# Kernel tuning notes

Measured on AMD Instinct MI355X. Metric: run time of the kernel, lower is better.

Reference implementation:

```python
import jax, jax.numpy as jnp
import numpy as np

D_MODEL = 1024
NHEAD = 16
HEAD_DIM = D_MODEL // NHEAD
EPS = 1e-5


def layernorm(x, g, b):
    mu = jnp.mean(x, axis=-1, keepdims=True)
    var = jnp.mean(jnp.square(x - mu), axis=-1, keepdims=True)
    return (x - mu) * jax.lax.rsqrt(var + EPS) * g + b


def setup_inputs() -> dict:
    key = jax.random.key(0)
    ks = jax.random.split(key, 10)
    B, S, D = 8, 2048, D_MODEL
    s = 1.0 / np.sqrt(D)
    return {
        "x": jax.random.normal(ks[0], (B, S, D), dtype=jnp.float32),
        "wq": jax.random.normal(ks[1], (D, D), dtype=jnp.float32) * s,
        "wk": jax.random.normal(ks[2], (D, D), dtype=jnp.float32) * s,
        "wv": jax.random.normal(ks[3], (D, D), dtype=jnp.float32) * s,
        "ln1_g": jnp.ones((D,), dtype=jnp.float32),
        "ln1_b": jnp.zeros((D,), dtype=jnp.float32),
        "ln2_g": jnp.ones((D,), dtype=jnp.float32),
        "ln2_b": jnp.zeros((D,), dtype=jnp.float32),
        "w1": jax.random.normal(ks[4], (D, D), dtype=jnp.float32) * s,
        "b1": jnp.zeros((D,), dtype=jnp.float32),
        "w2": jax.random.normal(ks[5], (D, D), dtype=jnp.float32) * s,
        "b2": jnp.zeros((D,), dtype=jnp.float32),
    }


def reference(x, wq, wk, wv, ln1_g, ln1_b, ln2_g, ln2_b, w1, b1, w2, b2):
    B, S, D = x.shape
    H, Dh = NHEAD, HEAD_DIM
    xn = layernorm(x, ln1_g, ln1_b)
    # nn.Linear: y = x @ W.T (no bias for q/k/v)
    q = (xn @ wq.T).reshape(B, S, H, Dh)
    k = (xn @ wk.T).reshape(B, S, H, Dh)
    v = (xn @ wv.T).reshape(B, S, H, Dh)
    scale = 1.0 / jnp.sqrt(jnp.float32(Dh))
    scores = jnp.einsum("bqhd,bkhd->bhqk", q, k) * scale  # [B,H,S,S]
    attn = jax.nn.softmax(scores, axis=-1)
    att = jnp.einsum("bhqk,bkhd->bqhd", attn, v).reshape(B, S, D)
    xt = layernorm(xn + att, ln2_g, ln2_b)
    ffn = jax.nn.relu(xt @ w1.T + b1) @ w2.T + b2
    return xt + ffn
```

## Files before the change

kernel.cpp:

```cpp
#include <hip/hip_runtime.h>
#include <hip/hip_bf16.h>

typedef __bf16 bf16x8 __attribute__((ext_vector_type(8)));
typedef float f32x4 __attribute__((ext_vector_type(4)));
typedef float f32x16 __attribute__((ext_vector_type(16)));

#define MFMA_B16(a, b, c) __builtin_amdgcn_mfma_f32_16x16x32_bf16((a), (b), (c), 0, 0, 0)
#define MFMA32_B16(a, b, c) __builtin_amdgcn_mfma_f32_32x32x16_bf16((a), (b), (c), 0, 0, 0)
#define GLD16(g, l)                                                              \
    __builtin_amdgcn_global_load_lds((__attribute__((address_space(1))) void*)(g), \
                                     (__attribute__((address_space(3))) void*)(l), \
                                     16, 0, 0)

__device__ __forceinline__ float bfu2f(unsigned short u) {
    return __uint_as_float(((unsigned)u) << 16);
}
__device__ __forceinline__ unsigned short f2bfu(float f) {
    unsigned u = __float_as_uint(f);
    u += 0x7fffu + ((u >> 16) & 1u);
    return (unsigned short)(u >> 16);
}
__device__ __forceinline__ float fexp2(float x) {
#if __has_builtin(__builtin_amdgcn_exp2f)
    return __builtin_amdgcn_exp2f(x);
#else
    return __expf(x * 0.69314718f);
#endif
}
__device__ __forceinline__ unsigned cvtpk_bf16(float lo_, float hi_) {
    unsigned r;
    asm("v_cvt_pk_bf16_f32 %0, %1, %2" : "=v"(r) : "v"(lo_), "v"(hi_));
    return r;
}
__device__ __forceinline__ void plswap(unsigned& a, unsigned& b) {
#if __has_builtin(__builtin_amdgcn_permlane32_swap)
    typedef int v2i __attribute__((ext_vector_type(2)));
    v2i r = __builtin_amdgcn_permlane32_swap((int)a, (int)b, false, false);
    a = (unsigned)r.x;
    b = (unsigned)r.y;
#else
    unsigned pa_ = (unsigned)__shfl_xor((int)a, 32);
    unsigned pb_ = (unsigned)__shfl_xor((int)b, 32);
    bool hi = (threadIdx.x & 63) >= 32;
    unsigned na = hi ? pb_ : a;
    unsigned nb = hi ? b : pa_;
    a = na;
    b = nb;
#endif
}

__global__ __launch_bounds__(256) void cvt5_f32_bf16(const float* __restrict__ s0,
                                                     const float* __restrict__ s1,
                                                     const float* __restrict__ s2,
                                                     const float* __restrict__ s3,
                                                     const float* __restrict__ s4,
                                                     unsigned short* __restrict__ dst) {
    int wsel = blockIdx.x >> 10;
    int i = (blockIdx.x & 1023) * 256 + threadIdx.x;
    const float* src = s0;
    if (wsel == 1) src = s1;
    else if (wsel == 2) src = s2;
    else if (wsel == 3) src = s3;
    else if (wsel == 4) src = s4;
    float4 v = ((const float4*)src)[i];
    ((ushort4*)dst)[wsel * 262144 + i] =
        make_ushort4(f2bfu(v.x), f2bfu(v.y), f2bfu(v.z), f2bfu(v.w));
}

__global__ __launch_bounds__(256) void ln1_kernel(const float* __restrict__ in1,
                                                  const float* __restrict__ gam,
                                                  const float* __restrict__ bet,
                                                  unsigned short* __restrict__ outb) {
    int row = blockIdx.x, tid = threadIdx.x;
    size_t base = (size_t)row * 1024 + tid * 4;
    float4 v = *(const float4*)(in1 + base);
    float s = v.x + v.y + v.z + v.w;
    float sq = v.x * v.x + v.y * v.y + v.z * v.z + v.w * v.w;
#pragma unroll
    for (int m = 1; m < 64; m <<= 1) {
        s += __shfl_xor(s, m);
        sq += __shfl_xor(sq, m);
    }
    __shared__ float red[8];
    int w = tid >> 6;
    if ((tid & 63) == 0) { red[w] = s; red[w + 4] = sq; }
    __syncthreads();
    s = red[0] + red[1] + red[2] + red[3];
    sq = red[4] + red[5] + red[6] + red[7];
    float mean = s * (1.0f / 1024.0f);
    float var = fmaxf(sq * (1.0f / 1024.0f) - mean * mean, 0.0f);
    float rstd = rsqrtf(var + 1e-5f);
    float4 g4 = *(const float4*)(gam + tid * 4);
    float4 b4 = *(const float4*)(bet + tid * 4);
    *(ushort4*)(outb + base) = make_ushort4(
        f2bfu((v.x - mean) * rstd * g4.x + b4.x), f2bfu((v.y - mean) * rstd * g4.y + b4.y),
        f2bfu((v.z - mean) * rstd * g4.z + b4.z), f2bfu((v.w - mean) * rstd * g4.w + b4.w));
}

__global__ __launch_bounds__(256) void ln2_kernel(const unsigned short* __restrict__ in1,
                                                  const unsigned short* __restrict__ in2,
                                                  const float* __restrict__ gam,
                                                  const float* __restrict__ bet,
                                                  unsigned short* __restrict__ outb) {
    int row = blockIdx.x, tid = threadIdx.x;
    size_t base = (size_t)row * 1024 + tid * 4;
    ushort4 a = *(const ushort4*)(in1 + base);
    ushort4 c = *(const ushort4*)(in2 + base);
    float4 v = make_float4(bfu2f(a.x) + bfu2f(c.x), bfu2f(a.y) + bfu2f(c.y),
                           bfu2f(a.z) + bfu2f(c.z), bfu2f(a.w) + bfu2f(c.w));
    float s = v.x + v.y + v.z + v.w;
    float sq = v.x * v.x + v.y * v.y + v.z * v.z + v.w * v.w;
#pragma unroll
    for (int m = 1; m < 64; m <<= 1) {
        s += __shfl_xor(s, m);
        sq += __shfl_xor(sq, m);
    }
    __shared__ float red[8];
    int w = tid >> 6;
    if ((tid & 63) == 0) { red[w] = s; red[w + 4] = sq; }
    __syncthreads();
    s = red[0] + red[1] + red[2] + red[3];
    sq = red[4] + red[5] + red[6] + red[7];
    float mean = s * (1.0f / 1024.0f);
    float var = fmaxf(sq * (1.0f / 1024.0f) - mean * mean, 0.0f);
    float rstd = rsqrtf(var + 1e-5f);
    float4 g4 = *(const float4*)(gam + tid * 4);
    float4 b4 = *(const float4*)(bet + tid * 4);
    *(ushort4*)(outb + base) = make_ushort4(
        f2bfu((v.x - mean) * rstd * g4.x + b4.x), f2bfu((v.y - mean) * rstd * g4.y + b4.y),
        f2bfu((v.z - mean) * rstd * g4.z + b4.z), f2bfu((v.w - mean) * rstd * g4.w + b4.w));
}

template <int MODE>
__global__ __launch_bounds__(512, 2) void gemm8(const unsigned short* __restrict__ A,
                                                const unsigned short* __restrict__ Bw,
                                                const float* __restrict__ bias,
                                                const unsigned short* __restrict__ resid,
                                                void* __restrict__ O0, void* __restrict__ O1,
                                                void* __restrict__ O2, int M, int N, int K) {
    __shared__ unsigned short As[4][8192];
    __shared__ unsigned short Bs[4][8192];
    int nt = N >> 8;
    int bid = blockIdx.x;
    int nwg = gridDim.x;
    int swz = (bid & 7) * (nwg >> 3) + (bid >> 3);
    int mt = swz / nt, ntl = swz % nt;
    int mbase = mt << 8, nbase = ntl << 8;
    int tid = threadIdx.x;
    int w = tid >> 6, l = tid & 63;
    int wm = w >> 2, wn = w & 3;
    int lr = l & 15, lg = l >> 4;
    int lx = lr & 7;
    int brow = (wn & 1) * 64;

    int srow = tid >> 3;
    int csrc = (tid & 7) ^ (srow & 7);
    const unsigned short* aRow = A + (size_t)(mbase + srow) * K + csrc * 8;
    const unsigned short* bRow = Bw + (size_t)(nbase + srow) * K + csrc * 8;

    const int NT = K >> 6;
    auto stA = [&](int buf, int h, int t) {
        if (t >= NT) return;
        const unsigned short* s0 = aRow + (size_t)(h * 128) * K + t * 64;
        GLD16(s0, &As[buf * 2 + h][w * 512]);
        GLD16(s0 + (size_t)64 * K, &As[buf * 2 + h][4096 + w * 512]);
    };
    auto stB = [&](int buf, int h, int t) {
        if (t >= NT) return;
        const unsigned short* s0 = bRow + (size_t)(h * 128) * K + t * 64;
        GLD16(s0, &Bs[buf * 2 + h][w * 512]);
        GLD16(s0 + (size_t)64 * K, &Bs[buf * 2 + h][4096 + w * 512]);
    };

    f32x4 acc[8][4] = {};
    bf16x8 afr[4][2], bq0[2][2], bq1[2][2];

    auto rdA = [&](int buf, int mq) {
        const unsigned short* base = &As[buf * 2 + wm][0];
#pragma unroll
        for (int mf = 0; mf < 4; mf++)
#pragma unroll
            for (int ks = 0; ks < 2; ks++)
                afr[mf][ks] = *(const bf16x8*)(base + (mq * 64 + mf * 16 + lr) * 64 +
                                               (((ks * 4 + lg) ^ lx) << 3));
    };
    auto rdB = [&](int buf, int nq, bf16x8 (&bf)[2][2]) {
        const unsigned short* base = &Bs[buf * 2 + (wn >> 1)][0];
#pragma unroll
        for (int nf = 0; nf < 2; nf++)
#pragma unroll
            for (int ks = 0; ks < 2; ks++)
                bf[nf][ks] = *(const bf16x8*)(base + (brow + nq * 32 + nf * 16 + lr) * 64 +
                                              (((ks * 4 + lg) ^ lx) << 3));
    };
    auto MM = [&](int mq, int nq, bf16x8 (&bf)[2][2]) {
        __builtin_amdgcn_s_setprio(1);
#pragma unroll
        for (int mf = 0; mf < 4; mf++)
#pragma unroll
            for (int nf = 0; nf < 2; nf++)
#pragma unroll
                for (int ks = 0; ks < 2; ks++)
                    acc[mq * 4 + mf][nq * 2 + nf] =
                        MFMA_B16(afr[mf][ks], bf[nf][ks], acc[mq * 4 + mf][nq * 2 + nf]);
        __builtin_amdgcn_s_setprio(0);
    };
#define BARX __builtin_amdgcn_s_barrier()
#define LGK0 do { asm volatile("s_waitcnt lgkmcnt(0)" ::: "memory"); \
                  __builtin_amdgcn_sched_barrier(0); } while (0)
#define VMC(n) asm volatile("s_waitcnt vmcnt(" #n ")" ::: "memory")

    stA(0, 0, 0); stA(0, 1, 0); stB(0, 0, 0); stB(0, 1, 0); stB(1, 0, 1); stB(1, 1, 1);
    VMC(4);
    BARX;

    int NIT = NT >> 1;
    for (int i = 0; i < NIT; i++) {
        int t0 = 2 * i, t1 = t0 + 1;
        bool lastI = (i == NIT - 1);
        rdA(0, 0); rdB(0, 0, bq0); stA(1, 0, t1);
        BARX; LGK0; MM(0, 0, bq0); BARX;
        rdB(0, 1, bq1); stA(1, 1, t1);
        BARX; LGK0; MM(0, 1, bq1); BARX;
        rdA(0, 1); stB(0, 0, t0 + 2);
        BARX; LGK0; MM(1, 1, bq1); BARX;
        stB(0, 1, t0 + 2);
        if (lastI) { VMC(0); } else { VMC(4); }
        BARX; MM(1, 0, bq0); BARX;
        rdA(1, 0); rdB(1, 0, bq0); stA(0, 0, t0 + 2);
        BARX; LGK0; MM(0, 0, bq0); BARX;
        rdB(1, 1, bq1); stA(0, 1, t0 + 2);
        BARX; LGK0; MM(0, 1, bq1); BARX;
        rdA(1, 1); stB(1, 0, t1 + 2);
        BARX; LGK0; MM(1, 1, bq1); BARX;
        stB(1, 1, t1 + 2);
        if (!lastI) { VMC(4); }
        BARX; MM(1, 0, bq0); BARX;
    }

#pragma unroll
    for (int m = 0; m < 8; m++) {
        int row = mbase + wm * 128 + (m >> 2) * 64 + (m & 3) * 16 + lg * 4;
#pragma unroll
        for (int n = 0; n < 4; n++) {
            int col = nbase + wn * 64 + (n >> 1) * 32 + (n & 1) * 16 + lr;
            if constexpr (MODE == 0) {
                int wsel = col >> 10;
                int cl = col & 1023;
                if (wsel == 2) {
                    int hh = cl >> 6, dd = cl & 63;
                    int bb = row >> 11, ss = row & 2047;
                    unsigned short t4[4];
#pragma unroll
                    for (int j = 0; j < 4; j++) t4[j] = f2bfu(acc[m][n][j]);
                    size_t vtidx = ((size_t)((bb * 16 + hh) * 64 + dd)) * 2048 + ss;
                    *(uint2*)((unsigned short*)O2 + vtidx) = *(uint2*)t4;
                } else {
                    unsigned short* out = (wsel == 0) ? (unsigned short*)O0 : (unsigned short*)O1;
                    float sc = (wsel == 0) ? 0.18033688f : 1.0f;
#pragma unroll
                    for (int j = 0; j < 4; j++)
                        out[(size_t)(row + j) * 1024 + cl] = f2bfu(acc[m][n][j] * sc);
                }
            } else {
                float bv = bias[col];
#pragma unroll
                for (int j = 0; j < 4; j++) {
                    float v = acc[m][n][j] + bv;
                    size_t idx = (size_t)(row + j) * N + col;
                    if constexpr (MODE == 1) {
                        ((unsigned short*)O0)[idx] = f2bfu(fmaxf(v, 0.0f));
                    } else {
                        ((float*)O0)[idx] = v + bfu2f(resid[idx]);
                    }
                }
            }
        }
    }
#undef BARX
#undef LGK0
#undef VMC
}

__global__ __launch_bounds__(512) void attn_kernel(const unsigned short* __restrict__ qq,
                                                   const unsigned short* __restrict__ kk,
                                                   const unsigned short* __restrict__ vT,
                                                   unsigned short* __restrict__ attb) {
    __shared__ unsigned short Ks[2][64 * 64];
    __shared__ unsigned short Vs[2][64 * 64];

    int bid = blockIdx.x;
    int swz = (bid & 7) * (gridDim.x >> 3) + (bid >> 3);
    int qi = swz & 7, h = (swz >> 3) & 15, b = swz >> 7;
    int tid = threadIdx.x, w = tid >> 6, l = tid & 63;
    int lo = l & 31, hi = l >> 5;
    int q0 = qi * 256 + w * 32;

    const unsigned short* qp = qq + ((size_t)((b * 2048 + q0 + lo) * 16 + h)) * 64 + hi * 8;
    bf16x8 qf[4];
#pragma unroll
    for (int kc = 0; kc < 4; kc++) qf[kc] = *(const bf16x8*)(qp + kc * 16);

    int srow = w * 8 + (l >> 3);
    int schunk = (l & 7) ^ ((l >> 3) & 7);
    const unsigned short* ksrc = kk + ((size_t)((b * 2048 + srow) * 16 + h)) * 64 + schunk * 8;
    const unsigned short* vsrc = vT + ((size_t)((b * 16 + h) * 64 + srow)) * 2048 + schunk * 8;

    f32x16 od0 = {}, od1 = {};
    float ssum = 0.f;

    GLD16(ksrc, &Ks[0][w * 512]);
    GLD16(vsrc, &Vs[0][w * 512]);
    ksrc += 65536;
    vsrc += 64;
    asm volatile("s_waitcnt vmcnt(0)");
    __syncthreads();

    int cur = 0;
    for (int t = 0; t < 32; t++) {
        if (t < 31) {
            GLD16(ksrc, &Ks[cur ^ 1][w * 512]);
            GLD16(vsrc, &Vs[cur ^ 1][w * 512]);
            ksrc += 65536;
            vsrc += 64;
        }
        const unsigned short* Kb = &Ks[cur][0];
        f32x16 sacc[2];
        __builtin_amdgcn_s_setprio(1);
#pragma unroll
        for (int tt = 0; tt < 2; tt++) {
            f32x16 s = {};
            int row = tt * 32 + lo;
#pragma unroll
            for (int kc = 0; kc < 4; kc++) {
                bf16x8 a = *(const bf16x8*)(Kb + row * 64 + (((kc * 2 + hi) ^ (row & 7)) << 3));
                s = MFMA32_B16(a, qf[kc], s);
            }
            sacc[tt] = s;
        }
        __builtin_amdgcn_s_setprio(0);
        float p[32];
        float psum = 0.f;
#pragma unroll
        for (int tt = 0; tt < 2; tt++)
#pragma unroll
            for (int r = 0; r < 16; r++) {
                float e = fexp2(sacc[tt][r]);
                p[tt * 16 + r] = e;
                psum += e;
            }
        psum += __shfl_xor(psum, 32);
        ssum += psum;
        const unsigned short* Vb = &Vs[cur][0];
#pragma unroll
        for (int tt = 0; tt < 2; tt++) {
            unsigned wv[8];
#pragma unroll
            for (int i = 0; i < 8; i++) wv[i] = cvtpk_bf16(p[tt * 16 + 2 * i], p[tt * 16 + 2 * i + 1]);
            plswap(wv[0], wv[2]);
            plswap(wv[1], wv[3]);
            plswap(wv[4], wv[6]);
            plswap(wv[5], wv[7]);
            union { unsigned u[4]; bf16x8 v; } c0, c1;
            c0.u[0] = wv[0]; c0.u[1] = wv[1]; c0.u[2] = wv[2]; c0.u[3] = wv[3];
            c1.u[0] = wv[4]; c1.u[1] = wv[5]; c1.u[2] = wv[6]; c1.u[3] = wv[7];
            __builtin_amdgcn_s_setprio(1);
#pragma unroll
            for (int sub = 0; sub < 2; sub++) {
                int ks = tt * 2 + sub;
                bf16x8 pa = sub ? c1.v : c0.v;
                int slot = ((ks * 2 + hi) ^ (lo & 7)) << 3;
                bf16x8 v0 = *(const bf16x8*)(Vb + lo * 64 + slot);
                bf16x8 v1 = *(const bf16x8*)(Vb + (32 + lo) * 64 + slot);
                od0 = MFMA32_B16(pa, v0, od0);
                od1 = MFMA32_B16(pa, v1, od1);
            }
            __builtin_amdgcn_s_setprio(0);
        }
        asm volatile("s_waitcnt vmcnt(0)");
        __syncthreads();
        cur ^= 1;
    }

#pragma unroll
    for (int r = 0; r < 16; r++) {
        int crow = (r & 3) + ((r >> 2) << 3) + (hi << 2);
        float rs = 1.0f / __shfl(ssum, crow);
        int q = q0 + crow;
        size_t base = ((size_t)((b * 2048 + q) * 16 + h)) * 64;
        attb[base + lo] = f2bfu(od0[r] * rs);
        attb[base + 32 + lo] = f2bfu(od1[r] * rs);
    }
}

extern "C" void kernel_launch(void* const* d_in, const int* in_sizes, int n_in,
                              void* d_out, int out_size, void* d_ws, size_t ws_size,
                              hipStream_t stream) {
    const float* x = (const float*)d_in[0];
    const float* wq = (const float*)d_in[1];
    const float* wk = (const float*)d_in[2];
    const float* wv = (const float*)d_in[3];
    const float* ln1_g = (const float*)d_in[4];
    const float* ln1_b = (const float*)d_in[5];
    const float* ln2_g = (const float*)d_in[6];
    const float* ln2_b = (const float*)d_in[7];
    const float* w1 = (const float*)d_in[8];
    const float* b1 = (const float*)d_in[9];
    const float* w2 = (const float*)d_in[10];
    const float* b2 = (const float*)d_in[11];

    const size_t NB = 33554432;
    char* ws = (char*)d_ws;
    unsigned short* xn_b = (unsigned short*)(ws);
    unsigned short* q_b = (unsigned short*)(ws + NB);
    unsigned short* k_b = (unsigned short*)(ws + 2 * NB);
    unsigned short* vT_b = (unsigned short*)(ws + 3 * NB);
    unsigned short* att_b = (unsigned short*)(ws + 4 * NB);
    unsigned short* wq_b = (unsigned short*)(ws + 5 * NB);
    unsigned short* w1_b = wq_b + 3145728;
    unsigned short* w2_b = w1_b + 1048576;
    unsigned short* xt_b = q_b;
    unsigned short* h_b = k_b;

    dim3 blk(256);
    cvt5_f32_bf16<<<5120, blk, 0, stream>>>(wq, wk, wv, w1, w2, wq_b);
    ln1_kernel<<<16384, blk, 0, stream>>>(x, ln1_g, ln1_b, xn_b);

    gemm8<0><<<768, dim3(512), 0, stream>>>(xn_b, wq_b, nullptr, nullptr,
                                            q_b, k_b, vT_b, 16384, 3072, 1024);

    attn_kernel<<<1024, dim3(512), 0, stream>>>(q_b, k_b, vT_b, att_b);

    ln2_kernel<<<16384, blk, 0, stream>>>(xn_b, att_b, ln2_g, ln2_b, xt_b);

    gemm8<1><<<256, dim3(512), 0, stream>>>(xt_b, w1_b, b1, nullptr,
                                            h_b, nullptr, nullptr, 16384, 1024, 1024);
    gemm8<2><<<256, dim3(512), 0, stream>>>(h_b, w2_b, b2, xt_b,
                                            d_out, nullptr, nullptr, 16384, 1024, 1024);
}
```

Measured before the change: 394.6 us.

## Deepen attention K/V prefetch to a 4-stage ring and stagger wave pairs

Replaces the double-buffered K/V LDS tiles in the attention kernel with a 4-deep ring that prefetches three tiles ahead. The old per-step full drain (vmcnt(0) plus syncthreads) becomes a partial vmcnt wait and a raw barrier. Odd waves work one tile ahead of even waves, wrapping to tile 0 at the end. This spreads MFMA and exp phases and LDS traffic across the wave pairs, and load latency is hidden deeper. In exchange the kernel doubles its LDS footprint and adds an extra barrier per step. The exp row-sum is also split into two accumulators to add ILP.

```diff
diff --git a/kernel.cpp b/kernel.cpp
--- a/kernel.cpp
+++ b/kernel.cpp
@@ -286,14 +286,15 @@
                                                    const unsigned short* __restrict__ kk,
                                                    const unsigned short* __restrict__ vT,
                                                    unsigned short* __restrict__ attb) {
-    __shared__ unsigned short Ks[2][64 * 64];
-    __shared__ unsigned short Vs[2][64 * 64];
+    __shared__ unsigned short Ks[4][64 * 64];
+    __shared__ unsigned short Vs[4][64 * 64];
 
     int bid = blockIdx.x;
     int swz = (bid & 7) * (gridDim.x >> 3) + (bid >> 3);
     int qi = swz & 7, h = (swz >> 3) & 15, b = swz >> 7;
     int tid = threadIdx.x, w = tid >> 6, l = tid & 63;
     int lo = l & 31, hi = l >> 5;
+    int g = w & 1;
     int q0 = qi * 256 + w * 32;
 
     const unsigned short* qp = qq + ((size_t)((b * 2048 + q0 + lo) * 16 + h)) * 64 + hi * 8;
@@ -303,55 +304,60 @@
 
     int srow = w * 8 + (l >> 3);
     int schunk = (l & 7) ^ ((l >> 3) & 7);
-    const unsigned short* ksrc = kk + ((size_t)((b * 2048 + srow) * 16 + h)) * 64 + schunk * 8;
-    const unsigned short* vsrc = vT + ((size_t)((b * 16 + h) * 64 + srow)) * 2048 + schunk * 8;
+    const unsigned short* ksrc0 = kk + ((size_t)((b * 2048 + srow) * 16 + h)) * 64 + schunk * 8;
+    const unsigned short* vsrc0 = vT + ((size_t)((b * 16 + h) * 64 + srow)) * 2048 + schunk * 8;
+
+    auto stageT = [&](int s) {
+        if (s > 32) return;
+        int tile = s & 31;
+        GLD16(ksrc0 + (size_t)tile * 65536, &Ks[s & 3][w * 512]);
+        GLD16(vsrc0 + (size_t)tile * 64, &Vs[s & 3][w * 512]);
+    };
 
     f32x16 od0 = {}, od1 = {};
     float ssum = 0.f;
 
-    GLD16(ksrc, &Ks[0][w * 512]);
-    GLD16(vsrc, &Vs[0][w * 512]);
-    ksrc += 65536;
-    vsrc += 64;
-    asm volatile("s_waitcnt vmcnt(0)");
-    __syncthreads();
-
-    int cur = 0;
-    for (int t = 0; t < 32; t++) {
-        if (t < 31) {
-            GLD16(ksrc, &Ks[cur ^ 1][w * 512]);
-            GLD16(vsrc, &Vs[cur ^ 1][w * 512]);
-            ksrc += 65536;
-            vsrc += 64;
-        }
-        const unsigned short* Kb = &Ks[cur][0];
+    stageT(0); stageT(1); stageT(2);
+
+    for (int s = 0; s < 32; s++) {
+        stageT(s + 3);
+        if (s < 30) asm volatile("s_waitcnt vmcnt(4)" ::: "memory");
+        else if (s == 30) asm volatile("s_waitcnt vmcnt(2)" ::: "memory");
+        else asm volatile("s_waitcnt vmcnt(0)" ::: "memory");
+        __builtin_amdgcn_s_barrier();
+
+        int mbuf = (s + g) & 3;
+        const unsigned short* Kb = &Ks[mbuf][0];
+        const unsigned short* Vb = &Vs[mbuf][0];
+
         f32x16 sacc[2];
         __builtin_amdgcn_s_setprio(1);
 #pragma unroll
         for (int tt = 0; tt < 2; tt++) {
-            f32x16 s = {};
+            f32x16 sv = {};
             int row = tt * 32 + lo;
 #pragma unroll
             for (int kc = 0; kc < 4; kc++) {
                 bf16x8 a = *(const bf16x8*)(Kb + row * 64 + (((kc * 2 + hi) ^ (row & 7)) << 3));
-                s = MFMA32_B16(a, qf[kc], s);
+                sv = MFMA32_B16(a, qf[kc], sv);
             }
-            sacc[tt] = s;
+            sacc[tt] = sv;
         }
         __builtin_amdgcn_s_setprio(0);
         float p[32];
-        float psum = 0.f;
-#pragma unroll
-        for (int tt = 0; tt < 2; tt++)
-#pragma unroll
-            for (int r = 0; r < 16; r++) {
-                float e = fexp2(sacc[tt][r]);
-                p[tt * 16 + r] = e;
-                psum += e;
-            }
+        float ps0 = 0.f, ps1 = 0.f;
+#pragma unroll
+        for (int r = 0; r < 16; r++) {
+            float e0 = fexp2(sacc[0][r]);
+            float e1 = fexp2(sacc[1][r]);
+            p[r] = e0;
+            p[16 + r] = e1;
+            ps0 += e0;
+            ps1 += e1;
+        }
+        float psum = ps0 + ps1;
         psum += __shfl_xor(psum, 32);
         ssum += psum;
-        const unsigned short* Vb = &Vs[cur][0];
 #pragma unroll
         for (int tt = 0; tt < 2; tt++) {
             unsigned wv[8];
@@ -377,9 +383,7 @@
             }
             __builtin_amdgcn_s_setprio(0);
         }
-        asm volatile("s_waitcnt vmcnt(0)");
-        __syncthreads();
-        cur ^= 1;
+        __builtin_amdgcn_s_barrier();
     }
 
 #pragma unroll
```

After: 382.6 us. 1.03x faster.
